# Kernel optimization log

Hardware: AMD Instinct MI355X
Metric: run time of the kernel (lower is better)

## Reference

```python
import jax, jax.numpy as jnp
import numpy as np

H, F, K, R = 8, 64, 10, 256  # num_heads, in_features, num_sines, num_realizations
B, L = 4, 2048


def setup_inputs() -> dict:
    key = jax.random.key(0)
    k1, k2, k3, k4, k5, k6 = jax.random.split(key, 6)
    return {
        "queries": jax.random.normal(k1, (B, L, H, F), dtype=jnp.float32),
        "keys": jax.random.normal(k2, (B, L, H, F), dtype=jnp.float32),
        "z": jax.random.normal(k3, (B, H, F, 2 * K, R), dtype=jnp.float32),
        "freqs": jax.random.normal(k4, (H, F, K), dtype=jnp.float32),
        "offsets": jax.random.normal(k5, (H, F, K), dtype=jnp.float32),
        "gains": jax.random.normal(k6, (H, F, K), dtype=jnp.float32),
    }


def reference(queries, keys, z, freqs, offsets, gains):
    h, f_dim, k_sines = freqs.shape
    length = queries.shape[1]
    r = z.shape[-1]
    # split positional / non-positional features (rest is empty here: key_dim == in_features)
    q_pos, q_rest = queries[..., :f_dim], queries[..., f_dim:]
    k_pos, k_rest = keys[..., :f_dim], keys[..., f_dim:]

    idx = jnp.arange(length, dtype=queries.dtype)  # linspace(0, L-1, L)
    fr = jax.nn.sigmoid(freqs)[:, :, None, :] / 2.0          # [H, F, 1, K]
    base = 2.0 * jnp.pi * fr * idx[None, None, :, None]       # [H, F, L, K]
    ph_q = base + offsets[:, :, None, :]
    ph_k = base
    # stack(cos, sin) on last axis then flatten -> interleaved cos0,sin0,... : [H, F, L, 2K]
    omega_q = jnp.stack([jnp.cos(ph_q), jnp.sin(ph_q)], axis=-1).reshape(h, f_dim, length, 2 * k_sines)
    omega_k = jnp.stack([jnp.cos(ph_k), jnp.sin(ph_k)], axis=-1).reshape(h, f_dim, length, 2 * k_sines)

    g = jnp.tile(jax.nn.softplus(gains), (1, 1, 2))           # [H, F, 2K] (block-repeated, as in torch .repeat)
    zs = z * g[None, :, :, :, None] / np.sqrt(r * f_dim).astype(np.float32)  # [B, H, F, 2K, R]

    # fused double contraction over f (in_features) and s (2K sines); equals
    # (omega @ z) permuted then multiplied by queries and summed over in_features
    qhat = jnp.einsum('hfls,bhfsr,blhf->blhr', omega_q, zs, q_pos)  # [B, L, H, R]
    khat = jnp.einsum('hfls,bhfsr,blhf->blhr', omega_k, zs, k_pos)

    qhat = jnp.concatenate([qhat, q_rest], axis=-1)
    khat = jnp.concatenate([khat, k_rest], axis=-1)
    return qhat, khat
```

## Files before the change

### kernel.cpp

```cpp
#include <hip/hip_runtime.h>
#include <math.h>


#define NH 8
#define NF 64
#define NK 10
#define NR 256
#define NB 4
#define NL 2048
#define KTOT 1280
#define BK 32
#define NCH (KTOT/BK)
#define NFRAG_B 16
#define WS_BPACK ((size_t)NB*NH*NCH*NFRAG_B*1024)
#define WS_TRIG  ((size_t)NH*NCH*2048*16*4)
#define WS_NEED2 (WS_BPACK + WS_TRIG)

typedef __attribute__((ext_vector_type(8))) short short8;
typedef __attribute__((ext_vector_type(4))) float f32x4;
typedef __attribute__((ext_vector_type(4))) unsigned int u32x4;
typedef __attribute__((ext_vector_type(2))) unsigned int u32x2;

static __device__ __forceinline__ unsigned short f2b(float f) {
    unsigned x = __float_as_uint(f);
    return (unsigned short)((x + 0x7FFFu + ((x >> 16) & 1u)) >> 16);
}
static __device__ __forceinline__ unsigned int pk2(float a, float b) {
    return (unsigned int)f2b(a) | ((unsigned int)f2b(b) << 16);
}
static __device__ __forceinline__ unsigned int cvtpk(float lo, float hi) {
    unsigned int r;
    asm("v_cvt_pk_bf16_f32 %0, %1, %2" : "=v"(r) : "v"(lo), "v"(hi));
    return r;
}
static __device__ __forceinline__ void gload_lds16(const void* g, void* l) {
    __builtin_amdgcn_global_load_lds(
        (const __attribute__((address_space(1))) unsigned int*)g,
        (__attribute__((address_space(3))) unsigned int*)l, 16, 0, 0);
}

__global__ __launch_bounds__(256)
void spe_prep(const float* __restrict__ z, const float* __restrict__ gains,
              unsigned char* __restrict__ bpack)
{
    __shared__ float s_g[NF*NK];
    const int ch  = blockIdx.x;
    const int bh  = blockIdx.y;
    const int h   = bh & 7;
    const int tid = threadIdx.x;
    for (int i = tid; i < NF*NK; i += 256)
        s_g[i] = log1pf(expf(gains[h*NF*NK + i])) * 0.0078125f;
    __syncthreads();
    const float* zb = z + (size_t)bh * KTOT * NR;
    unsigned char* dst = bpack + ((size_t)(bh*NCH + ch) * NFRAG_B) * 1024;
    #pragma unroll
    for (int it = 0; it < 4; ++it) {
        const int s  = tid + 256*it;
        const int fi = s >> 6;
        const int l  = s & 63;
        const int r  = fi*16 + (l & 15);
        const int k0 = ch*BK + (l >> 4)*8;
        u32x4 wv;
        #pragma unroll
        for (int jp = 0; jp < 4; ++jp) {
            const int ka = k0 + 2*jp, kb = ka + 1;
            const int fa = (ka*3277) >> 16; int sa = ka - fa*20; if (sa >= NK) sa -= NK;
            const int fb = (kb*3277) >> 16; int sb = kb - fb*20; if (sb >= NK) sb -= NK;
            const float va = zb[(size_t)ka*NR + r] * s_g[fa*NK + sa];
            const float vb = zb[(size_t)kb*NR + r] * s_g[fb*NK + sb];
            wv[jp] = pk2(va, vb);
        }
        *(u32x4*)(dst + (size_t)s*16) = wv;
    }
}

__global__ __launch_bounds__(256)
void spe_trig(const float* __restrict__ freqs, unsigned int* __restrict__ trig)
{
    const int t = blockIdx.x;
    const int h = blockIdx.y;
    const int tid = threadIdx.x;
    #pragma unroll
    for (int it = 0; it < 32; ++it) {
        const int site = tid + 256*it;
        const int l  = site >> 2;
        const int jg = site & 3;
        u32x4 wv;
        #pragma unroll
        for (int j = 0; j < 4; ++j) {
            const int kidx2 = t*16 + jg*4 + j;
            const float fv = freqs[h*640 + kidx2];
            const float fr = 0.5f / (1.0f + expf(-fv));
            const float x  = __builtin_amdgcn_fractf(fr * (float)l);
            wv[j] = pk2(__builtin_amdgcn_cosf(x), __builtin_amdgcn_sinf(x));
        }
        *(u32x4*)(trig + ((size_t)(h*NCH + t)*2048 + l)*16 + jg*4) = wv;
    }
}

#define OFF3_B   0
#define OFF3_A   32768
#define OFF3_POS 49152
#define OFF3_CS  65536
#define SMEM3_SZ 70656

__global__ __launch_bounds__(512, 4)
void spe_main3(const float* __restrict__ queries, const float* __restrict__ keys,
               const float* __restrict__ offsets,
               const unsigned char* __restrict__ bpack,
               const unsigned int* __restrict__ trig,
               float* __restrict__ out)
{
    __shared__ __attribute__((aligned(16))) unsigned char smem[SMEM3_SZ];
    const int tid  = threadIdx.x;
    const int lane = tid & 63;
    const int w    = tid >> 6;

    const int fb = blockIdx.x;
    const int h  = fb & 7;
    const int b  = (fb >> 3) & 3;
    const int l0 = (fb >> 5) * 64;
    const int bh = b*NH + h;

    float2* ld_cs = (float2*)(smem + OFF3_CS);
    unsigned short* pos_t = (unsigned short*)(smem + OFF3_POS);

    for (int i = tid; i < NF*NK; i += 512) {
        const float xo = __builtin_amdgcn_fractf(offsets[h*640 + i] * 0.15915494309189535f);
        ld_cs[i] = make_float2(__builtin_amdgcn_cosf(xo), __builtin_amdgcn_sinf(xo));
    }
    {
        const int r  = tid >> 2;
        const int f0 = (tid & 3) * 16;
        const int rl = r & 63;
        const float* src = (r < 64)
            ? queries + ((size_t)((b*NL + l0 + rl)*NH + h))*NF + f0
            : keys    + ((size_t)((b*NL + l0 + rl)*NH + h))*NF + f0;
        unsigned short* pdst = pos_t + ((r >> 6) << 12);
        #pragma unroll
        for (int j = 0; j < 4; ++j) {
            const float4 v = *(const float4*)(src + j*4);
            const int f = f0 + j*4;
            pdst[(f+0)*64 + rl] = f2b(v.x);
            pdst[(f+1)*64 + rl] = f2b(v.y);
            pdst[(f+2)*64 + rl] = f2b(v.z);
            pdst[(f+3)*64 + rl] = f2b(v.w);
        }
    }

    const unsigned char* bp = bpack + (size_t)bh * ((size_t)NCH*NFRAG_B*1024);
    const unsigned int*  tp = trig  + (size_t)h  * ((size_t)NCH*2048*16);

    const int wq   = w >> 2;
    const int wn   = w & 3;
    const size_t tstep = (size_t)2048*16;
    const unsigned int* tbase = tp + (size_t)(l0 + lane)*16 + wn*4;
    const int a_w  = ((wq*4 + (lane >> 4)) << 10) + ((wn*16 + (lane & 15)) << 4);
    const int fi0  = w * 2;

    u32x4 trCur = *(const u32x4*)(tbase);
    gload_lds16(bp + (size_t)fi0*1024 + lane*16,     smem + OFF3_B + (fi0  << 10));
    gload_lds16(bp + (size_t)(fi0+1)*1024 + lane*16, smem + OFF3_B + ((fi0+1) << 10));
    u32x4 trNxt = *(const u32x4*)(tbase + tstep);
    __syncthreads();

    f32x4 acc[4][4];
    #pragma unroll
    for (int mi = 0; mi < 4; ++mi)
        #pragma unroll
        for (int ni = 0; ni < 4; ++ni)
            acc[mi][ni] = (f32x4){0.f, 0.f, 0.f, 0.f};

    auto synthA = [&](int t, const u32x4 tr) -> u32x4 {
        u32x4 av;
        const int kb = t*16 + wn*4;
        #pragma unroll
        for (int p = 0; p < 4; ++p) {
            const int kidx = kb + p;
            const int f    = (kidx * 6554) >> 16;
            const float ck = __uint_as_float(tr[p] << 16);
            const float sk = __uint_as_float(tr[p] & 0xffff0000u);
            const float pv = __uint_as_float(((unsigned)pos_t[wq*4096 + f*64 + lane]) << 16);
            float c, s;
            if (wq == 0) {
                const float2 cs = ld_cs[kidx];
                c = ck*cs.x - sk*cs.y;
                s = sk*cs.x + ck*cs.y;
            } else { c = ck; s = sk; }
            av[p] = cvtpk(c*pv, s*pv);
        }
        return av;
    };

    u32x4 av = synthA(0, trCur);

    #pragma unroll 2
    for (int t = 0; t < NCH; ++t) {
        const int par = t & 1;

        *(u32x4*)(smem + OFF3_A + par*8192 + a_w) = av;
        asm volatile("s_waitcnt lgkmcnt(0)" ::: "memory");
        if (t == NCH-1) { asm volatile("s_waitcnt vmcnt(0)" ::: "memory"); }
        else            { asm volatile("s_waitcnt vmcnt(1)" ::: "memory"); }
        __builtin_amdgcn_sched_barrier(0);
        __builtin_amdgcn_s_barrier();
        __builtin_amdgcn_sched_barrier(0);

        if (t + 1 < NCH) {
            unsigned char* Bn = smem + OFF3_B + ((t+1) & 1)*16384;
            gload_lds16(bp + ((size_t)(t+1)*NFRAG_B + fi0)*1024 + lane*16,
                        Bn + (fi0 << 10));
            gload_lds16(bp + ((size_t)(t+1)*NFRAG_B + fi0+1)*1024 + lane*16,
                        Bn + ((fi0+1) << 10));
        }
        u32x4 trTmp;
        if (t + 2 < NCH) trTmp = *(const u32x4*)(tbase + (size_t)(t+2)*tstep);
        __builtin_amdgcn_sched_barrier(0);

        const unsigned char* Bc = smem + OFF3_B + par*16384;
        short8 bf[4];
        #pragma unroll
        for (int ni = 0; ni < 4; ++ni)
            bf[ni] = *(const short8*)(Bc + ((wn*4 + ni) << 10) + (lane << 4));

        if (t + 1 < NCH) av = synthA(t + 1, trNxt);

        #pragma unroll
        for (int mi = 0; mi < 4; ++mi) {
            const short8 af = *(const short8*)(smem + OFF3_A + par*8192
                                               + ((wq*4 + mi) << 10) + (lane << 4));
            #pragma unroll
            for (int ni = 0; ni < 4; ++ni)
                acc[mi][ni] = __builtin_amdgcn_mfma_f32_16x16x32_bf16(af, bf[ni], acc[mi][ni], 0, 0, 0);
        }
        if (t + 2 < NCH) trNxt = trTmp;
    }

    const size_t qk_off = (size_t)wq * ((size_t)NB*NL*NH*NR);
    const int row_l = (lane >> 4) * 4;
    const int col_r = lane & 15;
    #pragma unroll
    for (int mi = 0; mi < 4; ++mi) {
        const int lg = l0 + mi*16 + row_l;
        #pragma unroll
        for (int ni = 0; ni < 4; ++ni) {
            const int rg = wn*64 + ni*16 + col_r;
            const f32x4 v = acc[mi][ni];
            #pragma unroll
            for (int q = 0; q < 4; ++q)
                out[qk_off + ((size_t)((b*NL + lg + q)*NH + h))*NR + rg] = v[q];
        }
    }
}

#define OFF_B   0
#define OFF_A   49152
#define OFF_POS 57344
#define OFF_FR  73728
#define OFF_CO  76288
#define OFF_SO  78848
#define SMEM_SZ 81408

__global__ __launch_bounds__(512, 4)
void spe_main(const float* __restrict__ queries, const float* __restrict__ keys,
              const float* __restrict__ freqs, const float* __restrict__ offsets,
              const unsigned char* __restrict__ bpack, float* __restrict__ out)
{
    __shared__ __attribute__((aligned(16))) unsigned char smem[SMEM_SZ];
    const int tid  = threadIdx.x;
    const int lane = tid & 63;
    const int w    = tid >> 6;
    const int l0   = blockIdx.x * 64;
    const int bh   = blockIdx.y;
    const int b = bh >> 3, h = bh & 7;

    float* ld_fr = (float*)(smem + OFF_FR);
    float* ld_co = (float*)(smem + OFF_CO);
    float* ld_so = (float*)(smem + OFF_SO);
    unsigned short* pos_t = (unsigned short*)(smem + OFF_POS);

    for (int i = tid; i < NF*NK; i += 512) {
        const float fv = freqs[h*NF*NK + i];
        ld_fr[i] = 0.5f / (1.0f + expf(-fv));
        const float xo = __builtin_amdgcn_fractf(offsets[h*NF*NK + i] * 0.15915494309189535f);
        ld_co[i] = __builtin_amdgcn_cosf(xo);
        ld_so[i] = __builtin_amdgcn_sinf(xo);
    }
    {
        const int r  = tid >> 2;
        const int f0 = (tid & 3) * 16;
        const int rl = r & 63;
        const float* src = (r < 64)
            ? queries + ((size_t)((b*NL + l0 + rl)*NH + h))*NF + f0
            : keys    + ((size_t)((b*NL + l0 + rl)*NH + h))*NF + f0;
        unsigned short* pdst = pos_t + ((r >> 6) << 12);
        #pragma unroll
        for (int j = 0; j < 4; ++j) {
            const float4 v = *(const float4*)(src + j*4);
            const int f = f0 + j*4;
            pdst[(f+0)*64 + rl] = f2b(v.x);
            pdst[(f+1)*64 + rl] = f2b(v.y);
            pdst[(f+2)*64 + rl] = f2b(v.z);
            pdst[(f+3)*64 + rl] = f2b(v.w);
        }
    }
    __syncthreads();

    const unsigned char* bp = bpack + (size_t)bh * ((size_t)NCH*NFRAG_B*1024);
    const int fi0 = w*2;
    gload_lds16(bp + (size_t)fi0*1024 + lane*16,               smem + OFF_B + (fi0  <<10));
    gload_lds16(bp + (size_t)(fi0+1)*1024 + lane*16,           smem + OFF_B + ((fi0+1)<<10));
    gload_lds16(bp + (size_t)(NFRAG_B + fi0)*1024 + lane*16,   smem + OFF_B + 16384 + (fi0  <<10));
    gload_lds16(bp + (size_t)(NFRAG_B + fi0+1)*1024 + lane*16, smem + OFF_B + 16384 + ((fi0+1)<<10));

    const int wm = w >> 2, wn = w & 3;
    f32x4 acc[4][4];
    #pragma unroll
    for (int mi = 0; mi < 4; ++mi)
        #pragma unroll
        for (int ni = 0; ni < 4; ++ni)
            acc[mi][ni] = (f32x4){0.f, 0.f, 0.f, 0.f};

    const int rq   = ((w & 1) << 5) | (lane & 31);
    const int oct  = w >> 1;
    const int half = lane >> 5;
    const float lf = (float)(l0 + rq);
    const unsigned short* posq = pos_t;
    const unsigned short* posk = pos_t + 4096;
    const int aw_q = OFF_A + ((rq >> 4) << 10) + ((oct*16 + (rq & 15)) << 4) + (half << 3);
    const int aw_k = aw_q + 4096;

    auto synthA = [&](int t, u32x2& q01, u32x2& k01) {
        #pragma unroll
        for (int p = 0; p < 2; ++p) {
            const int kk   = t*BK + oct*8 + half*4 + p*2;
            const int f    = (kk*3277) >> 16;
            const int srem = kk - f*20;
            const int kidx = f*NK + (srem >> 1);
            const float x  = __builtin_amdgcn_fractf(ld_fr[kidx] * lf);
            const float ck = __builtin_amdgcn_cosf(x);
            const float sk = __builtin_amdgcn_sinf(x);
            const float co = ld_co[kidx], so = ld_so[kidx];
            const float cq = ck*co - sk*so;
            const float sq = sk*co + ck*so;
            const float pq = __uint_as_float(((unsigned)posq[f*64 + rq]) << 16);
            const float pk = __uint_as_float(((unsigned)posk[f*64 + rq]) << 16);
            q01[p] = cvtpk(cq*pq, sq*pq);
            k01[p] = cvtpk(ck*pk, sk*pk);
        }
    };

    u32x2 q01, k01;
    synthA(0, q01, k01);

    int bsel  = 0;
    int bsel2 = 2;
    for (int t = 0; t < NCH; ++t) {
        if (t < NCH-1) { asm volatile("s_waitcnt vmcnt(2)" ::: "memory"); }
        else           { asm volatile("s_waitcnt vmcnt(0)" ::: "memory"); }
        __builtin_amdgcn_sched_barrier(0);
        __builtin_amdgcn_s_barrier();

        if (t + 2 < NCH) {
            unsigned char* Bn = smem + OFF_B + bsel2*16384;
            gload_lds16(bp + (size_t)((t+2)*NFRAG_B + fi0)*1024 + lane*16,
                        Bn + (fi0<<10));
            gload_lds16(bp + (size_t)((t+2)*NFRAG_B + fi0+1)*1024 + lane*16,
                        Bn + ((fi0+1)<<10));
        }

        *(u32x2*)(smem + aw_q) = q01;
        *(u32x2*)(smem + aw_k) = k01;
        asm volatile("s_waitcnt lgkmcnt(0)" ::: "memory");
        __builtin_amdgcn_sched_barrier(0);
        __builtin_amdgcn_s_barrier();

        const unsigned char* Bc = smem + OFF_B + bsel*16384;
        short8 bf[4];
        #pragma unroll
        for (int ni = 0; ni < 4; ++ni)
            bf[ni] = *(const short8*)(Bc + ((wn*4 + ni) << 10) + (lane << 4));

        if (t + 1 < NCH) synthA(t + 1, q01, k01);

        #pragma unroll
        for (int mi = 0; mi < 4; ++mi) {
            const short8 af = *(const short8*)(smem + OFF_A + ((wm*4 + mi) << 10) + (lane << 4));
            #pragma unroll
            for (int ni = 0; ni < 4; ++ni)
                acc[mi][ni] = __builtin_amdgcn_mfma_f32_16x16x32_bf16(af, bf[ni], acc[mi][ni], 0, 0, 0);
        }

        bsel  = (bsel  == 2) ? 0 : bsel  + 1;
        bsel2 = (bsel2 == 2) ? 0 : bsel2 + 1;
    }

    const size_t qk_off = (size_t)wm * ((size_t)NB*NL*NH*NR);
    const int row_l = (lane >> 4) * 4;
    const int col_r = lane & 15;
    #pragma unroll
    for (int mi = 0; mi < 4; ++mi) {
        const int lg = l0 + mi*16 + row_l;
        #pragma unroll
        for (int ni = 0; ni < 4; ++ni) {
            const int rg = wn*64 + ni*16 + col_r;
            const f32x4 v = acc[mi][ni];
            #pragma unroll
            for (int q = 0; q < 4; ++q)
                out[qk_off + ((size_t)((b*NL + lg + q)*NH + h))*NR + rg] = v[q];
        }
    }
}

extern "C" void kernel_launch(void* const* d_in, const int* in_sizes, int n_in,
                              void* d_out, int out_size, void* d_ws, size_t ws_size,
                              hipStream_t stream) {
    const float* queries = (const float*)d_in[0];
    const float* keys    = (const float*)d_in[1];
    const float* z       = (const float*)d_in[2];
    const float* freqs   = (const float*)d_in[3];
    const float* offsets = (const float*)d_in[4];
    const float* gains   = (const float*)d_in[5];
    float* out = (float*)d_out;

    unsigned char* bpack = (unsigned char*)d_ws;
    spe_prep<<<dim3(NCH, NB*NH), 256, 0, stream>>>(z, gains, bpack);

    if (ws_size >= WS_NEED2) {
        unsigned int* trig = (unsigned int*)(bpack + WS_BPACK);
        spe_trig<<<dim3(NCH, NH), 256, 0, stream>>>(freqs, trig);
        spe_main3<<<dim3(1024), 512, 0, stream>>>(queries, keys, offsets, bpack, trig, out);
    } else {
        spe_main<<<dim3(NL/64, NB*NH), 512, 0, stream>>>(queries, keys, freqs, offsets, bpack, out);
    }
}
```

Baseline: 141.2 us.

## Load B fragments directly into registers instead of staging through LDS

The main GEMM kernel no longer stages the packed z (B operand) tiles through shared memory with async global-to-LDS copies. Each wave now loads its own four B fragments straight from global memory into registers, double-buffered as even and odd sets, with the loop manually unrolled by two. This cuts LDS use from about 70KB to 38KB and removes the vmcnt waits tied to the LDS copies. In exchange, each B fragment is fetched from global memory (mostly L2) by both wq waves instead of once per block, which adds register pressure and global traffic.

Result: slower. 148.8 us (+5.4%).

```diff
diff --git a/kernel.cpp b/kernel.cpp
--- a/kernel.cpp
+++ b/kernel.cpp
@@ -98,20 +98,19 @@
     }
 }
 
-#define OFF3_B   0
-#define OFF3_A   32768
-#define OFF3_POS 49152
-#define OFF3_CS  65536
-#define SMEM3_SZ 70656
+#define OFF4_A   0
+#define OFF4_POS 16384
+#define OFF4_CS  32768
+#define SMEM4_SZ 37888
 
 __global__ __launch_bounds__(512, 4)
-void spe_main3(const float* __restrict__ queries, const float* __restrict__ keys,
+void spe_main4(const float* __restrict__ queries, const float* __restrict__ keys,
                const float* __restrict__ offsets,
                const unsigned char* __restrict__ bpack,
                const unsigned int* __restrict__ trig,
                float* __restrict__ out)
 {
-    __shared__ __attribute__((aligned(16))) unsigned char smem[SMEM3_SZ];
+    __shared__ __attribute__((aligned(16))) unsigned char smem[SMEM4_SZ];
     const int tid  = threadIdx.x;
     const int lane = tid & 63;
     const int w    = tid >> 6;
@@ -122,8 +121,8 @@
     const int l0 = (fb >> 5) * 64;
     const int bh = b*NH + h;
 
-    float2* ld_cs = (float2*)(smem + OFF3_CS);
-    unsigned short* pos_t = (unsigned short*)(smem + OFF3_POS);
+    float2* ld_cs = (float2*)(smem + OFF4_CS);
+    unsigned short* pos_t = (unsigned short*)(smem + OFF4_POS);
 
     for (int i = tid; i < NF*NK; i += 512) {
         const float xo = __builtin_amdgcn_fractf(offsets[h*640 + i] * 0.15915494309189535f);
@@ -156,12 +155,14 @@
     const size_t tstep = (size_t)2048*16;
     const unsigned int* tbase = tp + (size_t)(l0 + lane)*16 + wn*4;
     const int a_w  = ((wq*4 + (lane >> 4)) << 10) + ((wn*16 + (lane & 15)) << 4);
-    const int fi0  = w * 2;
-
-    u32x4 trCur = *(const u32x4*)(tbase);
-    gload_lds16(bp + (size_t)fi0*1024 + lane*16,     smem + OFF3_B + (fi0  << 10));
-    gload_lds16(bp + (size_t)(fi0+1)*1024 + lane*16, smem + OFF3_B + ((fi0+1) << 10));
-    u32x4 trNxt = *(const u32x4*)(tbase + tstep);
+    const unsigned char* bwv = bp + (wn*4 << 10) + lane*16;
+
+    u32x4 trEven = *(const u32x4*)(tbase);
+    short8 bfEven[4], bfOdd[4];
+    #pragma unroll
+    for (int ni = 0; ni < 4; ++ni)
+        bfEven[ni] = *(const short8*)(bwv + (ni << 10));
+    u32x4 trOdd = *(const u32x4*)(tbase + tstep);
     __syncthreads();
 
     f32x4 acc[4][4];
@@ -172,7 +173,7 @@
             acc[mi][ni] = (f32x4){0.f, 0.f, 0.f, 0.f};
 
     auto synthA = [&](int t, const u32x4 tr) -> u32x4 {
-        u32x4 av;
+        u32x4 av_;
         const int kb = t*16 + wn*4;
         #pragma unroll
         for (int p = 0; p < 4; ++p) {
@@ -187,53 +188,45 @@
                 c = ck*cs.x - sk*cs.y;
                 s = sk*cs.x + ck*cs.y;
             } else { c = ck; s = sk; }
-            av[p] = cvtpk(c*pv, s*pv);
-        }
-        return av;
+            av_[p] = cvtpk(c*pv, s*pv);
+        }
+        return av_;
     };
 
-    u32x4 av = synthA(0, trCur);
-
-    #pragma unroll 2
-    for (int t = 0; t < NCH; ++t) {
-        const int par = t & 1;
-
-        *(u32x4*)(smem + OFF3_A + par*8192 + a_w) = av;
+    u32x4 av = synthA(0, trEven);
+
+    auto iter = [&](int t, int par, short8 (&bfC)[4], short8 (&bfN)[4],
+                    const u32x4 trUse, u32x4& trLoad) {
+        *(u32x4*)(smem + OFF4_A + par*8192 + a_w) = av;
         asm volatile("s_waitcnt lgkmcnt(0)" ::: "memory");
-        if (t == NCH-1) { asm volatile("s_waitcnt vmcnt(0)" ::: "memory"); }
-        else            { asm volatile("s_waitcnt vmcnt(1)" ::: "memory"); }
         __builtin_amdgcn_sched_barrier(0);
         __builtin_amdgcn_s_barrier();
-        __builtin_amdgcn_sched_barrier(0);
 
         if (t + 1 < NCH) {
-            unsigned char* Bn = smem + OFF3_B + ((t+1) & 1)*16384;
-            gload_lds16(bp + ((size_t)(t+1)*NFRAG_B + fi0)*1024 + lane*16,
-                        Bn + (fi0 << 10));
-            gload_lds16(bp + ((size_t)(t+1)*NFRAG_B + fi0+1)*1024 + lane*16,
-                        Bn + ((fi0+1) << 10));
-        }
-        u32x4 trTmp;
-        if (t + 2 < NCH) trTmp = *(const u32x4*)(tbase + (size_t)(t+2)*tstep);
-        __builtin_amdgcn_sched_barrier(0);
-
-        const unsigned char* Bc = smem + OFF3_B + par*16384;
-        short8 bf[4];
-        #pragma unroll
-        for (int ni = 0; ni < 4; ++ni)
-            bf[ni] = *(const short8*)(Bc + ((wn*4 + ni) << 10) + (lane << 4));
-
-        if (t + 1 < NCH) av = synthA(t + 1, trNxt);
+            const unsigned char* bn = bwv + (size_t)(t+1)*16384;
+            #pragma unroll
+            for (int ni = 0; ni < 4; ++ni)
+                bfN[ni] = *(const short8*)(bn + (ni << 10));
+        }
+        if (t + 2 < NCH)
+            trLoad = *(const u32x4*)(tbase + (size_t)(t+2)*tstep);
+
+        if (t + 1 < NCH) av = synthA(t + 1, trUse);
 
         #pragma unroll
         for (int mi = 0; mi < 4; ++mi) {
-            const short8 af = *(const short8*)(smem + OFF3_A + par*8192
+            const short8 af = *(const short8*)(smem + OFF4_A + par*8192
                                                + ((wq*4 + mi) << 10) + (lane << 4));
             #pragma unroll
             for (int ni = 0; ni < 4; ++ni)
-                acc[mi][ni] = __builtin_amdgcn_mfma_f32_16x16x32_bf16(af, bf[ni], acc[mi][ni], 0, 0, 0);
-        }
-        if (t + 2 < NCH) trNxt = trTmp;
+                acc[mi][ni] = __builtin_amdgcn_mfma_f32_16x16x32_bf16(af, bfC[ni], acc[mi][ni], 0, 0, 0);
+        }
+    };
+
+    #pragma unroll 1
+    for (int t = 0; t < NCH; t += 2) {
+        iter(t,     0, bfEven, bfOdd,  trOdd,  trEven);
+        iter(t + 1, 1, bfOdd,  bfEven, trEven, trOdd);
     }
 
     const size_t qk_off = (size_t)wq * ((size_t)NB*NL*NH*NR);
@@ -429,7 +422,7 @@
     if (ws_size >= WS_NEED2) {
         unsigned int* trig = (unsigned int*)(bpack + WS_BPACK);
         spe_trig<<<dim3(NCH, NH), 256, 0, stream>>>(freqs, trig);
-        spe_main3<<<dim3(1024), 512, 0, stream>>>(queries, keys, offsets, bpack, trig, out);
+        spe_main4<<<dim3(1024), 512, 0, stream>>>(queries, keys, offsets, bpack, trig, out);
     } else {
         spe_main<<<dim3(NL/64, NB*NH), 512, 0, stream>>>(queries, keys, freqs, offsets, bpack, out);
     }
```
